# Performance work log

Measured on AMD Instinct MI355X. Metric: run time of the kernel, lower is better.

The kernel has to match this reference:

```python
import jax, jax.numpy as jnp
import numpy as np

B, S, E, H = 2, 2048, 1024, 16
HD = E // H


def setup_inputs() -> dict:
    key = jax.random.key(0)
    ks = jax.random.split(key, 9)
    s = 1.0 / np.sqrt(E)
    return {
        "x": jax.random.normal(ks[0], (B, S, E), dtype=jnp.float32),
        "wq": jax.random.uniform(ks[1], (E, E), jnp.float32, -s, s),
        "bq": jax.random.uniform(ks[2], (E,), jnp.float32, -s, s),
        "wk": jax.random.uniform(ks[3], (E, E), jnp.float32, -s, s),
        "bk": jax.random.uniform(ks[4], (E,), jnp.float32, -s, s),
        "wv": jax.random.uniform(ks[5], (E, E), jnp.float32, -s, s),
        "bv": jax.random.uniform(ks[6], (E,), jnp.float32, -s, s),
        "wo": jax.random.uniform(ks[7], (E, E), jnp.float32, -s, s),
        "bo": jax.random.uniform(ks[8], (E,), jnp.float32, -s, s),
    }


def reference(x, wq, bq, wk, bk, wv, bv, wo, bo):
    b, s, e = x.shape
    # QKV projections, reshape to [b, h, s, hd]
    def proj(w, bias):
        y = jnp.einsum('bse,ef->bsf', x, w.T) + bias
        return y.reshape(b, s, H, HD).transpose(0, 2, 1, 3)
    q = proj(wq, bq)
    k = proj(wk, bk)
    v = proj(wv, bv)
    score = jnp.einsum('bhqd,bhkd->bhqk', q, k) / jnp.sqrt(jnp.float32(HD))
    # original: exp(x)/sum(exp(x)) + 1e-8  == softmax(x) + 1e-8
    attn = jax.nn.softmax(score, axis=-1) + 1e-8
    out = jnp.einsum('bhqk,bhkd->bhqd', attn, v)
    out = out.transpose(0, 2, 1, 3).reshape(b, s, e)
    return jnp.einsum('bse,ef->bsf', out, wo.T) + bo
```

## Files before the change

### kernel.cpp

```cpp
#include <hip/hip_runtime.h>
#include <hip/hip_bf16.h>
#include <cstdint>

#define SS 2048
#define EE 1024
#define HH 16
#define HDD 64

typedef __attribute__((ext_vector_type(8))) __bf16 bf16x8;
typedef __attribute__((ext_vector_type(4))) float f32x4;

#define MFMA16(a, b, c) __builtin_amdgcn_mfma_f32_16x16x32_bf16((a), (b), (c), 0, 0, 0)

__device__ __forceinline__ unsigned short f2bf(float f) {
    unsigned int u = __builtin_bit_cast(unsigned int, f);
    u += 0x7FFFu + ((u >> 16) & 1u);
    return (unsigned short)(u >> 16);
}

__device__ __forceinline__ void gll16(const unsigned short* g, unsigned short* l) {
    __builtin_amdgcn_global_load_lds(
        (__attribute__((address_space(1))) unsigned int*)g,
        (__attribute__((address_space(3))) unsigned int*)l, 16, 0, 0);
}

__device__ __forceinline__ void pl32swap(unsigned int& a, unsigned int& b) {
#if __has_builtin(__builtin_amdgcn_permlane32_swap)
    auto r = __builtin_amdgcn_permlane32_swap(a, b, false, false);
    a = r[0]; b = r[1];
#else
    unsigned int as = __shfl_xor(a, 32, 64), bs = __shfl_xor(b, 32, 64);
    const bool hi = (threadIdx.x & 32) != 0;
    unsigned int na = hi ? bs : a, nb = hi ? b : as;
    a = na; b = nb;
#endif
}

__device__ __forceinline__ void pl16swap(unsigned int& a, unsigned int& b) {
#if __has_builtin(__builtin_amdgcn_permlane16_swap)
    auto r = __builtin_amdgcn_permlane16_swap(a, b, false, false);
    a = r[0]; b = r[1];
#else
    unsigned int as = __shfl_xor(a, 16, 64), bs = __shfl_xor(b, 16, 64);
    const bool odd = (threadIdx.x & 16) != 0;
    unsigned int na = odd ? bs : a, nb = odd ? b : as;
    a = na; b = nb;
#endif
}

__global__ __launch_bounds__(256) void cvt_all(
    const float* __restrict__ x, const float* __restrict__ wq, const float* __restrict__ wk,
    const float* __restrict__ wv, const float* __restrict__ wo,
    unsigned short* __restrict__ xb, unsigned short* __restrict__ wqb, unsigned short* __restrict__ wkb,
    unsigned short* __restrict__ wvb, unsigned short* __restrict__ wob) {
    int idx = blockIdx.x * 256 + threadIdx.x;
    int i4 = idx << 2;
    const float* src;
    unsigned short* dst;
    int off;
    if (i4 < 4194304) { src = x; dst = xb; off = i4; }
    else {
        int w = (i4 - 4194304) >> 20;
        off = (i4 - 4194304) & 1048575;
        if (w == 0) { src = wq; dst = wqb; }
        else if (w == 1) { src = wk; dst = wkb; }
        else if (w == 2) { src = wv; dst = wvb; }
        else { src = wo; dst = wob; }
    }
    float4 v = *(const float4*)&src[off];
    unsigned int p0 = (unsigned int)f2bf(v.x) | ((unsigned int)f2bf(v.y) << 16);
    unsigned int p1 = (unsigned int)f2bf(v.z) | ((unsigned int)f2bf(v.w) << 16);
    uint2 u; u.x = p0; u.y = p1;
    *(uint2*)&dst[off] = u;
}

template <int MODE, int BMT, int BNT>
__device__ __forceinline__ void gemm_core(
    unsigned short* __restrict__ lsA,
    unsigned short* __restrict__ lsB,
    const unsigned short* __restrict__ A, const unsigned short* __restrict__ W,
    const float* __restrict__ bias, void* __restrict__ out, int bm, int bn) {
    constexpr int IT = BMT / 32, JT = BNT / 32;
    constexpr int ASTR = BMT * 32, BSTR = BNT * 32;
    const int t = threadIdx.x;
    const int lane = t & 63, l15 = lane & 15, quad = lane >> 4;
    const int wave = t >> 6;
    const int wm = (wave >> 1) * (BMT / 2), wn = (wave & 1) * (BNT / 2);

    const int cg = ((t & 3) ^ ((t >> 3) & 3)) * 8;
    const unsigned short* ga = A + (size_t)(bm + (t >> 2)) * 1024 + cg;
    const unsigned short* gb = W + (size_t)(bn + (t >> 2)) * 1024 + cg;

    f32x4 acc[IT][JT];
    for (int i = 0; i < IT; i++)
        for (int j = 0; j < JT; j++) acc[i][j] = (f32x4){0.f, 0.f, 0.f, 0.f};

    const int swz = (l15 >> 1) & 3;

    gll16(ga, &lsA[t * 8]);
    if (BMT == 128) gll16(ga + 64 * 1024, &lsA[2048 + t * 8]);
    gll16(gb, &lsB[t * 8]);
    if (BNT == 128) gll16(gb + 64 * 1024, &lsB[2048 + t * 8]);

    for (int it = 0; it < 32; it++) {
        const int cur = it & 1, nxt = cur ^ 1;
        __syncthreads();

        if (it < 31) {
            const int k0 = (it + 1) * 32;
            gll16(ga + k0, &lsA[nxt * ASTR + t * 8]);
            if (BMT == 128) gll16(ga + k0 + 64 * 1024, &lsA[nxt * ASTR + 2048 + t * 8]);
            gll16(gb + k0, &lsB[nxt * BSTR + t * 8]);
            if (BNT == 128) gll16(gb + k0 + 64 * 1024, &lsB[nxt * BSTR + 2048 + t * 8]);
        }

        bf16x8 af[IT], bfr[JT];
        for (int i = 0; i < IT; i++)
            af[i] = *(const bf16x8*)&lsA[cur * ASTR + (wm + i * 16 + l15) * 32 + ((quad ^ swz) * 8)];
        for (int j = 0; j < JT; j++)
            bfr[j] = *(const bf16x8*)&lsB[cur * BSTR + (wn + j * 16 + l15) * 32 + ((quad ^ swz) * 8)];
        for (int i = 0; i < IT; i++)
            for (int j = 0; j < JT; j++) acc[i][j] = MFMA16(af[i], bfr[j], acc[i][j]);
    }

    for (int j = 0; j < JT; j++) {
        int n = bn + wn + j * 16 + l15;
        float bj = bias[n];
        for (int i = 0; i < IT; i++) {
            int m0 = bm + wm + i * 16 + quad * 4;
            int srow0 = m0 & 2047, bidx = m0 >> 11;
            if (MODE == 3) {
                size_t headb = ((size_t)bidx * HH + (n >> 6)) * (SS * HDD);
                size_t base = headb + (size_t)(srow0 >> 6) * 4096 +
                              (size_t)(((srow0 >> 4) & 3) * 8 + ((n & 63) >> 3)) * 128 + (n & 7);
                for (int rg = 0; rg < 4; rg++)
                    ((unsigned short*)out)[base + (size_t)((srow0 & 15) + rg) * 8] = f2bf(acc[i][j][rg] + bj);
            } else if (MODE == 4) {
                size_t headb = ((size_t)bidx * HH + (n >> 6)) * (SS * HDD);
                size_t addr = headb + (size_t)(srow0 >> 6) * 4096 + (size_t)((n & 63) >> 4) * 1024 +
                              (size_t)(((srow0 >> 5) & 1) * 4 + ((srow0 >> 3) & 3)) * 128 +
                              (size_t)(n & 15) * 8 + (srow0 & 7);
                float v0 = acc[i][j][0] + bj, v1 = acc[i][j][1] + bj;
                float v2 = acc[i][j][2] + bj, v3 = acc[i][j][3] + bj;
                uint2 w;
                w.x = (unsigned int)f2bf(v0) | ((unsigned int)f2bf(v1) << 16);
                w.y = (unsigned int)f2bf(v2) | ((unsigned int)f2bf(v3) << 16);
                *(uint2*)&((unsigned short*)out)[addr] = w;
            } else {
                for (int rg = 0; rg < 4; rg++) {
                    float val = acc[i][j][rg] + bj;
                    int m = m0 + rg;
                    if (MODE == 0) {
                        ((unsigned short*)out)[(((size_t)(m >> 11) * HH + (n >> 6)) * SS + (m & 2047)) * HDD + (n & 63)] = f2bf(val);
                    } else {
                        ((float*)out)[(size_t)m * 1024 + n] = val;
                    }
                }
            }
        }
    }
}

__global__ __launch_bounds__(256) void gemm_qkv(
    const unsigned short* __restrict__ xb,
    const unsigned short* __restrict__ wqb, const unsigned short* __restrict__ wkb,
    const unsigned short* __restrict__ wvb,
    const float* __restrict__ bq, const float* __restrict__ bk, const float* __restrict__ bv,
    unsigned short* qb, unsigned short* kb, unsigned short* vtb) {
    __shared__ unsigned short shA[2 * 4096];
    __shared__ unsigned short shB[2 * 4096];
    const int blk = blockIdx.x;
    const int u = blk & 7, r = blk >> 3;
    const int by = u + 8 * (r & 3);
    const int rest = r >> 2;
    const int bx = rest & 7, z = rest >> 3;
    if (z == 0)      gemm_core<0, 128, 128>(shA, shB, xb, wqb, bq, qb,  by * 128, bx * 128);
    else if (z == 1) gemm_core<3, 128, 128>(shA, shB, xb, wkb, bk, kb,  by * 128, bx * 128);
    else             gemm_core<4, 128, 128>(shA, shB, xb, wvb, bv, vtb, by * 128, bx * 128);
}

__global__ __launch_bounds__(256) void gemm_out(
    const unsigned short* __restrict__ ob, const unsigned short* __restrict__ wob,
    const float* __restrict__ bo, float* __restrict__ out) {
    __shared__ unsigned short shA[2 * 4096];
    __shared__ unsigned short shB[2 * 2048];
    const int blk = blockIdx.x;
    const int u = blk & 7, r = blk >> 3;
    const int by = u + 8 * (r & 3);
    const int bx = r >> 2;
    gemm_core<1, 128, 64>(shA, shB, ob, wob, bo, out, by * 128, bx * 64);
}

__global__ __launch_bounds__(512, 4) void attn_fwd(
    const unsigned short* __restrict__ qb, const unsigned short* __restrict__ kb,
    const unsigned short* __restrict__ vtb, unsigned short* __restrict__ ob) {
    __shared__ unsigned short sh[32768];
    unsigned short* lsK = sh;
    unsigned short* lsV = sh + 16384;
    const int t = threadIdx.x, lane = t & 63, l15 = lane & 15, quad = lane >> 4;
    const int wave = t >> 6;
    const int half = wave >> 2;
    const int wq = wave & 3;
    const int tg = t & 255;
    const int blk = blockIdx.x;
    const int u = blk & 7, r = blk >> 3;
    const int bh = u + 8 * (r & 3);
    const int qt = r >> 2;
    const size_t hoff = (size_t)bh * (SS * HDD);
    const float C = 0.125f * 1.44269504088896f;

    bf16x8 qf[2][2];
    const int qrow = qt * 128 + wq * 32;
    for (int i = 0; i < 2; i++)
        for (int ks = 0; ks < 2; ks++) {
            bf16x8 raw = *(const bf16x8*)&qb[hoff + (size_t)(qrow + i * 16 + l15) * HDD + ks * 32 + quad * 8];
            unsigned short tmp[8];
            *(bf16x8*)tmp = raw;
            for (int j = 0; j < 8; j++) {
                float f = __builtin_bit_cast(float, (unsigned int)tmp[j] << 16);
                tmp[j] = f2bf(f * C);
            }
            qf[i][ks] = *(const bf16x8*)tmp;
        }

    unsigned short onesbuf[8];
    for (int j = 0; j < 8; j++) onesbuf[j] = 0x3F80;
    const bf16x8 onesf = *(const bf16x8*)onesbuf;

    f32x4 lacc[2];
    f32x4 o[2][4];
    for (int i = 0; i < 2; i++) {
        lacc[i] = (f32x4){0.f, 0.f, 0.f, 0.f};
        for (int jh = 0; jh < 4; jh++) o[i][jh] = (f32x4){0.f, 0.f, 0.f, 0.f};
    }

    const unsigned short* gk = kb + hoff + (size_t)half * 16 * 4096;
    const unsigned short* gv = vtb + hoff + (size_t)half * 16 * 4096;
    const int foff = quad * 128 + l15 * 8;

    auto stage = [&](int buf, int tile) {
        unsigned short* dk = lsK + buf * 8192 + half * 4096;
        unsigned short* dv = lsV + buf * 8192 + half * 4096;
        const unsigned short* sk = gk + tile * 4096;
        const unsigned short* sv = gv + tile * 4096;
        gll16(sk + tg * 8, dk + tg * 8);
        gll16(sk + 2048 + tg * 8, dk + 2048 + tg * 8);
        gll16(sv + tg * 8, dv + tg * 8);
        gll16(sv + 2048 + tg * 8, dv + 2048 + tg * 8);
    };

    stage(0, 0);

    for (int kt = 0; kt < 16; kt++) {
        const int cur = kt & 1;
        __syncthreads();

        if (kt < 15) stage(cur ^ 1, kt + 1);

        const unsigned short* myK = lsK + cur * 8192 + half * 4096;
        const unsigned short* myV = lsV + cur * 8192 + half * 4096;

        bf16x8 kfr[4][2];
        for (int j = 0; j < 4; j++)
            for (int ks = 0; ks < 2; ks++)
                kfr[j][ks] = *(const bf16x8*)&myK[j * 1024 + ks * 512 + foff];

        f32x4 st[2][4];
        for (int j = 0; j < 4; j++)
            for (int i = 0; i < 2; i++) {
                f32x4 z = (f32x4){0.f, 0.f, 0.f, 0.f};
                z = MFMA16(kfr[j][0], qf[i][0], z);
                z = MFMA16(kfr[j][1], qf[i][1], z);
                st[i][j] = z;
            }

        bf16x8 pf[2][2];
        for (int i = 0; i < 2; i++) {
            unsigned int W[4][2];
            for (int j = 0; j < 4; j++) {
                float e0 = __builtin_amdgcn_exp2f(st[i][j][0]);
                float e1 = __builtin_amdgcn_exp2f(st[i][j][1]);
                float e2 = __builtin_amdgcn_exp2f(st[i][j][2]);
                float e3 = __builtin_amdgcn_exp2f(st[i][j][3]);
                W[j][0] = (__builtin_bit_cast(unsigned int, e0) >> 16) |
                          (__builtin_bit_cast(unsigned int, e1) & 0xFFFF0000u);
                W[j][1] = (__builtin_bit_cast(unsigned int, e2) >> 16) |
                          (__builtin_bit_cast(unsigned int, e3) & 0xFFFF0000u);
            }

            unsigned int P0[4], P1[4];
            for (int h = 0; h < 2; h++) {
                unsigned int x = W[0][h], y = W[1][h];
                pl32swap(x, y);
                pl16swap(x, y);
                P0[h] = x; P0[2 + h] = y;
                unsigned int x2 = W[2][h], y2 = W[3][h];
                pl32swap(x2, y2);
                pl16swap(x2, y2);
                P1[h] = x2; P1[2 + h] = y2;
            }
            union { unsigned int u4[4]; bf16x8 v; } cv0, cv1;
            for (int p = 0; p < 4; p++) { cv0.u4[p] = P0[p]; cv1.u4[p] = P1[p]; }
            pf[i][0] = cv0.v;
            pf[i][1] = cv1.v;
        }

        for (int jh = 0; jh < 4; jh++) {
            bf16x8 v0 = *(const bf16x8*)&myV[jh * 1024 + foff];
            bf16x8 v1 = *(const bf16x8*)&myV[jh * 1024 + 512 + foff];
            for (int i = 0; i < 2; i++) {
                o[i][jh] = MFMA16(pf[i][0], v0, o[i][jh]);
                o[i][jh] = MFMA16(pf[i][1], v1, o[i][jh]);
            }
        }
        for (int i = 0; i < 2; i++) {
            lacc[i] = MFMA16(pf[i][0], onesf, lacc[i]);
            lacc[i] = MFMA16(pf[i][1], onesf, lacc[i]);
        }
    }

    __syncthreads();
    float* cb = (float*)sh;
    float* lb = cb + 8192;
    const int lslot = wq * 64 + lane;
    if (half == 1) {
        for (int i = 0; i < 2; i++)
            for (int jh = 0; jh < 4; jh++)
                for (int rg = 0; rg < 4; rg++)
                    cb[(i * 16 + jh * 4 + rg) * 256 + lslot] = o[i][jh][rg];
        for (int i = 0; i < 2; i++)
            for (int rg = 0; rg < 4; rg++)
                lb[(i * 4 + rg) * 256 + lslot] = lacc[i][rg];
    }
    __syncthreads();
    if (half == 0) {
        const int b = bh >> 4, h = bh & 15;
        for (int i = 0; i < 2; i++)
            for (int rg = 0; rg < 4; rg++) {
                float inv = 1.f / (lacc[i][rg] + lb[(i * 4 + rg) * 256 + lslot]);
                int srow = qrow + i * 16 + quad * 4 + rg;
                size_t rowoff = ((size_t)b * SS + srow) * EE + h * 64;
                for (int jh = 0; jh < 4; jh++) {
                    float val = o[i][jh][rg] + cb[(i * 16 + jh * 4 + rg) * 256 + lslot];
                    ob[rowoff + jh * 16 + l15] = f2bf(val * inv);
                }
            }
    }
}

extern "C" void kernel_launch(void* const* d_in, const int* in_sizes, int n_in,
                              void* d_out, int out_size, void* d_ws, size_t ws_size,
                              hipStream_t stream) {
    const float* x  = (const float*)d_in[0];
    const float* wq = (const float*)d_in[1];
    const float* bq = (const float*)d_in[2];
    const float* wk = (const float*)d_in[3];
    const float* bk = (const float*)d_in[4];
    const float* wv = (const float*)d_in[5];
    const float* bv = (const float*)d_in[6];
    const float* wo = (const float*)d_in[7];
    const float* bo = (const float*)d_in[8];

    char* ws = (char*)d_ws;
    unsigned short* xb  = (unsigned short*)(ws + 0);
    unsigned short* wqb = (unsigned short*)(ws + 8388608);
    unsigned short* wkb = (unsigned short*)(ws + 10485760);
    unsigned short* wvb = (unsigned short*)(ws + 12582912);
    unsigned short* wob = (unsigned short*)(ws + 14680064);
    unsigned short* qb  = (unsigned short*)(ws + 16777216);
    unsigned short* kb  = (unsigned short*)(ws + 25165824);
    unsigned short* vtb = (unsigned short*)(ws + 33554432);
    unsigned short* ob  = xb;

    cvt_all<<<8192, 256, 0, stream>>>(x, wq, wk, wv, wo, xb, wqb, wkb, wvb, wob);
    gemm_qkv<<<768, 256, 0, stream>>>(xb, wqb, wkb, wvb, bq, bk, bv, qb, kb, vtb);
    attn_fwd<<<512, 512, 0, stream>>>(qb, kb, vtb, ob);
    gemm_out<<<512, 256, 0, stream>>>(ob, wob, bo, (float*)d_out);
}
```

Before: 187.8 us.

## Software-pipeline attention loop so PV of previous tile overlaps QK of current

Splits the attention inner loop into QK/exp/pack, V-fragment read and PV stages. The loop is restructured so each iteration issues the PV MFMAs for the previous tile before the QK MFMAs and exp work for the current tile. P and V fragments are carried across iterations in registers, with a prologue and an epilogue. This is meant to let the scheduler interleave exp/permute ALU work with MFMA work and hide LDS read latency, at the cost of extra live registers that could lower occupancy.

```diff
diff --git a/kernel.cpp b/kernel.cpp
--- a/kernel.cpp
+++ b/kernel.cpp
@@ -249,22 +249,14 @@
         gll16(sv + 2048 + tg * 8, dv + 2048 + tg * 8);
     };
 
-    stage(0, 0);
-
-    for (int kt = 0; kt < 16; kt++) {
-        const int cur = kt & 1;
-        __syncthreads();
-
-        if (kt < 15) stage(cur ^ 1, kt + 1);
-
-        const unsigned short* myK = lsK + cur * 8192 + half * 4096;
-        const unsigned short* myV = lsV + cur * 8192 + half * 4096;
-
+    bf16x8 pfp[2][2];
+    bf16x8 vfp[4][2];
+
+    auto qk_pack = [&](const unsigned short* myK) {
         bf16x8 kfr[4][2];
         for (int j = 0; j < 4; j++)
             for (int ks = 0; ks < 2; ks++)
                 kfr[j][ks] = *(const bf16x8*)&myK[j * 1024 + ks * 512 + foff];
-
         f32x4 st[2][4];
         for (int j = 0; j < 4; j++)
             for (int i = 0; i < 2; i++) {
@@ -273,8 +265,6 @@
                 z = MFMA16(kfr[j][1], qf[i][1], z);
                 st[i][j] = z;
             }
-
-        bf16x8 pf[2][2];
         for (int i = 0; i < 2; i++) {
             unsigned int W[4][2];
             for (int j = 0; j < 4; j++) {
@@ -287,7 +277,6 @@
                 W[j][1] = (__builtin_bit_cast(unsigned int, e2) >> 16) |
                           (__builtin_bit_cast(unsigned int, e3) & 0xFFFF0000u);
             }
-
             unsigned int P0[4], P1[4];
             for (int h = 0; h < 2; h++) {
                 unsigned int x = W[0][h], y = W[1][h];
@@ -301,23 +290,46 @@
             }
             union { unsigned int u4[4]; bf16x8 v; } cv0, cv1;
             for (int p = 0; p < 4; p++) { cv0.u4[p] = P0[p]; cv1.u4[p] = P1[p]; }
-            pf[i][0] = cv0.v;
-            pf[i][1] = cv1.v;
-        }
-
+            pfp[i][0] = cv0.v;
+            pfp[i][1] = cv1.v;
+        }
+    };
+    auto readV = [&](const unsigned short* myV) {
         for (int jh = 0; jh < 4; jh++) {
-            bf16x8 v0 = *(const bf16x8*)&myV[jh * 1024 + foff];
-            bf16x8 v1 = *(const bf16x8*)&myV[jh * 1024 + 512 + foff];
+            vfp[jh][0] = *(const bf16x8*)&myV[jh * 1024 + foff];
+            vfp[jh][1] = *(const bf16x8*)&myV[jh * 1024 + 512 + foff];
+        }
+    };
+    auto pv = [&]() {
+        for (int jh = 0; jh < 4; jh++)
             for (int i = 0; i < 2; i++) {
-                o[i][jh] = MFMA16(pf[i][0], v0, o[i][jh]);
-                o[i][jh] = MFMA16(pf[i][1], v1, o[i][jh]);
-            }
-        }
+                o[i][jh] = MFMA16(pfp[i][0], vfp[jh][0], o[i][jh]);
+                o[i][jh] = MFMA16(pfp[i][1], vfp[jh][1], o[i][jh]);
+            }
         for (int i = 0; i < 2; i++) {
-            lacc[i] = MFMA16(pf[i][0], onesf, lacc[i]);
-            lacc[i] = MFMA16(pf[i][1], onesf, lacc[i]);
-        }
-    }
+            lacc[i] = MFMA16(pfp[i][0], onesf, lacc[i]);
+            lacc[i] = MFMA16(pfp[i][1], onesf, lacc[i]);
+        }
+    };
+
+    stage(0, 0);
+
+    __syncthreads();
+    stage(1, 1);
+    qk_pack(lsK + half * 4096);
+    readV(lsV + half * 4096);
+
+    for (int kt = 1; kt < 16; kt++) {
+        const int cur = kt & 1;
+        __syncthreads();
+        if (kt < 15) stage(cur ^ 1, kt + 1);
+        pv();
+        const unsigned short* myK = lsK + cur * 8192 + half * 4096;
+        const unsigned short* myV = lsV + cur * 8192 + half * 4096;
+        qk_pack(myK);
+        readV(myV);
+    }
+    pv();
 
     __syncthreads();
     float* cb = (float*)sh;
```

Result: no change. 188.4 us (+0.3%).
